# Optimization experiments

Measured on AMD Instinct MI355X. Metric: run time of the kernel, lower is better.

The kernel has to match this reference:

```python
import jax, jax.numpy as jnp
import numpy as np

MODEL_DIM = 2048
Q_HEADS = 32
KV_HEADS = 8
HEAD_DIM = MODEL_DIM // Q_HEADS  # 64
ROPE_BASE = 10000.0


def apply_rope(x, pos):
    # x: [B, S, H, D], interleaved-pair RoPE (torchtune-style)
    half = x.shape[-1] // 2
    inv_freq = 1.0 / (ROPE_BASE ** (jnp.arange(half, dtype=jnp.float32) * 2.0 / x.shape[-1]))
    ang = pos.astype(jnp.float32)[:, None] * inv_freq[None, :]        # [S, half]
    cos = jnp.cos(ang)[None, :, None, :]                              # [1,S,1,half]
    sin = jnp.sin(ang)[None, :, None, :]
    x1 = x[..., 0::2]
    x2 = x[..., 1::2]
    o1 = x1 * cos - x2 * sin
    o2 = x2 * cos + x1 * sin
    return jnp.stack([o1, o2], axis=-1).reshape(x.shape)


def setup_inputs() -> dict:
    key = jax.random.key(0)
    ks = jax.random.split(key, 5)
    B, S, D = 2, 2048, MODEL_DIM
    sd = 1.0 / np.sqrt(D)
    x = jax.random.normal(ks[0], (B, S, D), dtype=jnp.float32)
    wq = jax.random.normal(ks[1], (Q_HEADS * HEAD_DIM, D), dtype=jnp.float32) * sd
    wk = jax.random.normal(ks[2], (KV_HEADS * HEAD_DIM, D), dtype=jnp.float32) * sd
    wv = jax.random.normal(ks[3], (KV_HEADS * HEAD_DIM, D), dtype=jnp.float32) * sd
    wo = jax.random.normal(ks[4], (D, D), dtype=jnp.float32) * sd
    attention_mask = jnp.ones((B, S), dtype=bool)
    return {"x": x, "attention_mask": attention_mask, "wq": wq, "wk": wk, "wv": wv, "wo": wo}


def reference(x, attention_mask, wq, wk, wv, wo):
    B, S, D = x.shape
    rep = Q_HEADS // KV_HEADS
    q = (x @ wq.T).reshape(B, S, Q_HEADS, HEAD_DIM)
    k = (x @ wk.T).reshape(B, S, KV_HEADS, HEAD_DIM)
    v = (x @ wv.T).reshape(B, S, KV_HEADS, HEAD_DIM)
    # GQA repeat_interleave along head axis
    k = jnp.repeat(k, rep, axis=2)
    v = jnp.repeat(v, rep, axis=2)
    pos = jnp.arange(S)
    q = apply_rope(q, pos)
    k = apply_rope(k, pos)
    # scores [B, H, Sq, Sk]
    score = jnp.einsum('bqhd,bkhd->bhqk', q, k) / np.sqrt(HEAD_DIM)
    neg_inf = jnp.finfo(score.dtype).min
    causal = jnp.tril(jnp.ones((S, S), dtype=bool))
    score = jnp.where(causal[None, None, :, :], score, neg_inf)
    score = jnp.where(attention_mask[:, None, None, :], score, neg_inf)
    attn = jax.nn.softmax(score, axis=-1)
    out = jnp.einsum('bhqk,bkhd->bqhd', attn, v).reshape(B, S, D)
    return out @ wo.T
```

## Files before the change

### kernel.cpp

```cpp
#include <hip/hip_runtime.h>
#include <hip/hip_bf16.h>

#define S_LEN 2048
#define BATCH 2
#define DMODEL 2048
#define HQ 32
#define HKV 8
#define HD 64
#define NQ 2560
#define KDIM 2048

typedef __attribute__((ext_vector_type(8))) short bf16x8;
typedef __attribute__((ext_vector_type(4))) float f32x4;

#if __has_builtin(__builtin_amdgcn_exp2f)
#define EXP2(x) __builtin_amdgcn_exp2f(x)
#else
#define EXP2(x) exp2f(x)
#endif

template<int N> struct ic { static constexpr int value = N; };

static __device__ inline ushort f2bf(float f) {
    union { float f; unsigned u; } v; v.f = f;
    unsigned r = v.u + 0x7fff + ((v.u >> 16) & 1);
    return (ushort)(r >> 16);
}
static __device__ inline float bf2f(ushort h) {
    union { unsigned u; float f; } v; v.u = ((unsigned)h) << 16; return v.f;
}
static __device__ inline unsigned pack2(float lo, float hi) {
    return (unsigned)f2bf(lo) | ((unsigned)f2bf(hi) << 16);
}
static __device__ __forceinline__ unsigned pkbf(float lo, float hi) {
    union { float f; unsigned u; } a, b; a.f = lo; b.f = hi;
    return __builtin_amdgcn_perm(b.u + 0x8000u, a.u + 0x8000u, 0x07060302u);
}
static __device__ __forceinline__ unsigned cvtpk(float lo, float hi) {
    unsigned r;
    asm("v_cvt_pk_bf16_f32 %0, %1, %2" : "=v"(r) : "v"(lo), "v"(hi));
    return r;
}

static __device__ __forceinline__ void gload16(const ushort* g, ushort* l) {
    __builtin_amdgcn_global_load_lds(
        (const __attribute__((address_space(1))) unsigned int*)(g),
        (__attribute__((address_space(3))) unsigned int*)(l), 16, 0, 0);
}

#define BARRIER() asm volatile("s_barrier" ::: "memory")
#define WAITVM(N) asm volatile("s_waitcnt vmcnt(" #N ")" ::: "memory")

__global__ __launch_bounds__(256) void convert_kernel(const float* __restrict__ x,
                                                      const float* __restrict__ wq,
                                                      const float* __restrict__ wk,
                                                      const float* __restrict__ wv,
                                                      const float* __restrict__ wo,
                                                      ushort* __restrict__ xb,
                                                      ushort* __restrict__ wqkvb,
                                                      ushort* __restrict__ wob)
{
    size_t e = ((size_t)blockIdx.x * 256 + threadIdx.x) * 8;
    const float* src; ushort* dst;
    if (e < 8388608ul)       { src = x  + e;              dst = xb + e; }
    else if (e < 12582912ul) { src = wq + (e - 8388608);  dst = wqkvb + (e - 8388608); }
    else if (e < 13631488ul) { src = wk + (e - 12582912); dst = wqkvb + 4194304 + (e - 12582912); }
    else if (e < 14680064ul) { src = wv + (e - 13631488); dst = wqkvb + 5242880 + (e - 13631488); }
    else                     { src = wo + (e - 14680064); dst = wob + (e - 14680064); }
    float4 a = *(const float4*)src;
    float4 b = *(const float4*)(src + 4);
    uint4 p; p.x = pack2(a.x, a.y); p.y = pack2(a.z, a.w);
             p.z = pack2(b.x, b.y); p.w = pack2(b.z, b.w);
    *(uint4*)dst = p;
}

template<int BNF, int EPI>
__global__ __launch_bounds__(512, 2) void gemm256(const ushort* __restrict__ A,
                                                  const ushort* __restrict__ Bw,
                                                  ushort* __restrict__ qkv,
                                                  ushort* __restrict__ vT,
                                                  float* __restrict__ Cf)
{
    constexpr int BN = BNF * 64;
    constexpr int KT = KDIM / 64;
    __shared__ ushort As[2][256 * 64];
    __shared__ ushort Bs[2][BN * 64];
    const int t    = threadIdx.x;
    const int w    = t >> 6, lane = t & 63;
    const int quad = lane >> 4, l15 = lane & 15;
    const int l8   = lane >> 3;
    const int scw  = ((lane & 7) ^ (l8 & 7)) * 8;
    const int wm   = (w >> 2) * 128;
    const int wn   = (w & 3) * (BNF * 16);

    const int bid = blockIdx.x;
    const int sb  = (bid & 7) * 32 + (bid >> 3);
    const int mb  = (sb >> 4) * 256;
    const int nb  = (sb & 15) * BN;

    f32x4 acc[8][BNF] = {};
    bf16x8 a[4][2], b[BNF][2];

    auto SAH = [&](int buf, int half, int kb) {
        #pragma unroll
        for (int L = 0; L < 2; L++) {
            int r0 = half * 128 + (w * 2 + L) * 8;
            gload16(A + (size_t)(mb + r0 + l8) * KDIM + kb + scw, &As[buf][r0 * 64]);
        }
    };
    auto SB = [&](int buf, int kb) {
        #pragma unroll
        for (int L = 0; L < BNF; L++) {
            int r0 = (w * BNF + L) * 8;
            gload16(Bw + (size_t)(nb + r0 + l8) * KDIM + kb + scw, &Bs[buf][r0 * 64]);
        }
    };
    auto LA = [&](int buf, int hm) {
        #pragma unroll
        for (int i = 0; i < 4; i++) {
            int r = wm + hm * 64 + i * 16 + l15;
            int rs = r * 64, sw = r & 7;
            #pragma unroll
            for (int kc = 0; kc < 2; kc++)
                a[i][kc] = *(const bf16x8*)&As[buf][rs + (((kc << 2) | quad) ^ sw) * 8];
        }
    };
    auto LB = [&](int buf) {
        #pragma unroll
        for (int j = 0; j < BNF; j++) {
            int r = wn + j * 16 + l15;
            int rs = r * 64, sw = r & 7;
            #pragma unroll
            for (int kc = 0; kc < 2; kc++)
                b[j][kc] = *(const bf16x8*)&Bs[buf][rs + (((kc << 2) | quad) ^ sw) * 8];
        }
    };
    auto MM = [&](auto HM) {
        constexpr int hm = decltype(HM)::value;
        __builtin_amdgcn_s_setprio(1);
        #pragma unroll
        for (int i = 0; i < 4; i++)
            #pragma unroll
            for (int j = 0; j < BNF; j++) {
                f32x4 d = acc[hm * 4 + i][j];
                d = __builtin_amdgcn_mfma_f32_16x16x32_bf16(a[i][0], b[j][0], d, 0, 0, 0);
                d = __builtin_amdgcn_mfma_f32_16x16x32_bf16(a[i][1], b[j][1], d, 0, 0, 0);
                acc[hm * 4 + i][j] = d;
            }
        __builtin_amdgcn_s_setprio(0);
    };

    SAH(0, 0, 0); SAH(0, 1, 0); SB(0, 0);
    SAH(1, 0, 64); SB(1, 64);
    if constexpr (BNF == 3) WAITVM(5); else WAITVM(4);
    BARRIER();

    #pragma unroll 1
    for (int tt = 0; tt < KT - 2; tt++) {
        const int buf = tt & 1, o = buf ^ 1;
        LA(buf, 0); LB(buf);
        SAH(o, 1, (tt + 1) * 64);
        BARRIER();
        MM(ic<0>{});
        if constexpr (BNF == 3) WAITVM(7); else WAITVM(6);
        BARRIER();
        LA(buf, 1);
        SAH(buf, 0, (tt + 2) * 64); SB(buf, (tt + 2) * 64);
        BARRIER();
        MM(ic<1>{});
        if constexpr (BNF == 3) WAITVM(7); else WAITVM(6);
        BARRIER();
    }
    LA(0, 0); LB(0);
    SAH(1, 1, (KT - 1) * 64);
    BARRIER();
    MM(ic<0>{});
    if constexpr (BNF == 3) WAITVM(7); else WAITVM(6);
    BARRIER();
    LA(0, 1);
    BARRIER();
    MM(ic<1>{});
    WAITVM(2);
    BARRIER();
    LA(1, 0); LB(1);
    BARRIER();
    MM(ic<0>{});
    WAITVM(0);
    BARRIER();
    LA(1, 1);
    BARRIER();
    MM(ic<1>{});

    #pragma unroll
    for (int i = 0; i < 8; i++) {
        int m0 = mb + wm + (i >> 2) * 64 + (i & 3) * 16 + quad * 4;
        #pragma unroll
        for (int j = 0; j < BNF; j++) {
            int n0 = nb + wn + j * 16;
            if (EPI == 0) {
                if (n0 >= 2560) {
                    int m0p = (m0 & ~63) | (((m0 >> 5) & 1) << 5)
                            | (((m0 >> 2) & 3) << 3) | (((m0 >> 4) & 1) << 2);
                    ushort4 pk;
                    pk.x = f2bf(acc[i][j][0]); pk.y = f2bf(acc[i][j][1]);
                    pk.z = f2bf(acc[i][j][2]); pk.w = f2bf(acc[i][j][3]);
                    *(ushort4*)&vT[(size_t)(n0 + l15 - 2560) * 4096 + m0p] = pk;
                } else {
                    #pragma unroll
                    for (int r = 0; r < 4; r++)
                        qkv[(size_t)(m0 + r) * NQ + n0 + l15] = f2bf(acc[i][j][r]);
                }
            } else {
                #pragma unroll
                for (int r = 0; r < 4; r++)
                    Cf[(size_t)(m0 + r) * DMODEL + n0 + l15] = acc[i][j][r];
            }
        }
    }
}

__global__ __launch_bounds__(256) void rope_kernel(ushort* __restrict__ qkv)
{
    const int PAIRS = BATCH * S_LEN * (HQ + HKV) * (HD / 2);
    int tid = blockIdx.x * 256 + threadIdx.x;
    if (tid >= PAIRS) return;
    int token = tid / ((HQ + HKV) * 32);
    int r     = tid - token * ((HQ + HKV) * 32);
    int hh    = r >> 5;
    int i     = r & 31;
    int base  = (hh < HQ) ? hh * 64 : DMODEL + (hh - HQ) * 64;
    size_t addr = (size_t)token * NQ + base + 2 * i;
    int s = token & (S_LEN - 1);
    float freq = exp2f(-0.41524101186092f * (float)i);
    float ang  = (float)s * freq;
    float sn, cs;
    sincosf(ang, &sn, &cs);
    float x1 = bf2f(qkv[addr]);
    float x2 = bf2f(qkv[addr + 1]);
    qkv[addr]     = f2bf(x1 * cs - x2 * sn);
    qkv[addr + 1] = f2bf(x2 * cs + x1 * sn);
}

__global__ __launch_bounds__(256) void attn_kernel(const ushort* __restrict__ qkv,
                                                   const ushort* __restrict__ vT,
                                                   ushort* __restrict__ attnb)
{
    __shared__ ushort Ks[2][2 * 64 * 64];
    __shared__ ushort VT[2][2 * 64 * 64];
    const int t    = threadIdx.x;
    const int w    = t >> 6, lane = t & 63;
    const int quad = lane >> 4, l15 = lane & 15;
    const int bid  = blockIdx.x;
    const int qx   = 15 - (bid >> 6);
    const int h    = bid & 31;
    const int b    = (bid >> 5) & 1;
    const int qb   = qx * 128;
    const int kvh  = h >> 2;
    const ushort* base = qkv + (size_t)b * S_LEN * NQ;
    const ushort* vTb  = vT + (size_t)kvh * HD * 4096 + b * S_LEN;

    const float SC = 0.18033688011112042f;
    bf16x8 aq[2][2];
    #pragma unroll
    for (int h2 = 0; h2 < 2; h2++) {
        const ushort* qp = base + (size_t)(qb + w * 32 + h2 * 16 + l15) * NQ + h * HD + quad * 8;
        #pragma unroll
        for (int hf = 0; hf < 2; hf++) {
            bf16x8 v = *(const bf16x8*)(qp + hf * 32);
            #pragma unroll
            for (int j = 0; j < 8; j++) v[j] = (short)f2bf(bf2f((ushort)v[j]) * SC);
            aq[h2][hf] = v;
        }
    }

    f32x4 o[2][4] = {};
    float lsum[2] = {};
    const int qw    = qb + w * 32;
    const int strow = lane >> 3;
    const int stlc  = (lane & 7) ^ strow;
    const int niter = qx + 1;

    auto stage = [&](int i, int buf) {
        #pragma unroll
        for (int c = 0; c < 4; c++) {
            int key = w * 32 + c * 8 + strow;
            gload16(base + (size_t)(i * 128 + key) * NQ + DMODEL + kvh * HD + stlc * 8,
                    &Ks[buf][(w * 32 + c * 8) * 64]);
        }
        #pragma unroll
        for (int s = 0; s < 2; s++)
            #pragma unroll
            for (int c = 0; c < 2; c++) {
                int dr = w * 16 + c * 8 + strow;
                gload16(vTb + (size_t)dr * 4096 + i * 128 + s * 64 + stlc * 8,
                        &VT[buf][s * 4096 + (w * 16 + c * 8) * 64]);
            }
    };

    auto compute = [&](const ushort* ks, const ushort* vs, int kb) {
        const bool full = (kb + 63) <= qw;
        f32x4 s[2][4];
        __builtin_amdgcn_s_setprio(1);
        #pragma unroll
        for (int kt = 0; kt < 4; kt++) {
            int key = kt * 16 + l15;
            int sw  = l15 & 7;
            bf16x8 k0 = *(const bf16x8*)&ks[key * 64 + (quad ^ sw) * 8];
            bf16x8 k1 = *(const bf16x8*)&ks[key * 64 + (((quad + 4) & 7) ^ sw) * 8];
            #pragma unroll
            for (int h2 = 0; h2 < 2; h2++) {
                f32x4 z = {};
                z = __builtin_amdgcn_mfma_f32_16x16x32_bf16(k0, aq[h2][0], z, 0, 0, 0);
                z = __builtin_amdgcn_mfma_f32_16x16x32_bf16(k1, aq[h2][1], z, 0, 0, 0);
                s[h2][kt] = z;
            }
        }
        __builtin_amdgcn_s_setprio(0);
        bf16x8 pf[2][2];
        #pragma unroll
        for (int h2 = 0; h2 < 2; h2++) {
            union { unsigned u[8]; bf16x8 v[2]; } pw;
            #pragma unroll
            for (int kt = 0; kt < 4; kt++) {
                float p0 = EXP2(s[h2][kt][0]);
                float p1 = EXP2(s[h2][kt][1]);
                float p2 = EXP2(s[h2][kt][2]);
                float p3 = EXP2(s[h2][kt][3]);
                if (!full) {
                    int key0 = kb + kt * 16 + quad * 4;
                    int q    = qb + w * 32 + h2 * 16 + l15;
                    p0 = (key0 + 0 <= q) ? p0 : 0.f;
                    p1 = (key0 + 1 <= q) ? p1 : 0.f;
                    p2 = (key0 + 2 <= q) ? p2 : 0.f;
                    p3 = (key0 + 3 <= q) ? p3 : 0.f;
                }
                lsum[h2] += (p0 + p1) + (p2 + p3);
                pw.u[kt * 2 + 0] = cvtpk(p0, p1);
                pw.u[kt * 2 + 1] = cvtpk(p2, p3);
            }
            pf[h2][0] = pw.v[0];
            pf[h2][1] = pw.v[1];
        }
        __builtin_amdgcn_s_setprio(1);
        #pragma unroll
        for (int tt = 0; tt < 4; tt++) {
            int dr = tt * 16 + l15;
            int sw = l15 & 7;
            bf16x8 vf0 = *(const bf16x8*)&vs[dr * 64 + (quad ^ sw) * 8];
            bf16x8 vf1 = *(const bf16x8*)&vs[dr * 64 + (((quad + 4) & 7) ^ sw) * 8];
            #pragma unroll
            for (int h2 = 0; h2 < 2; h2++) {
                f32x4 oo = o[h2][tt];
                oo = __builtin_amdgcn_mfma_f32_16x16x32_bf16(vf0, pf[h2][0], oo, 0, 0, 0);
                oo = __builtin_amdgcn_mfma_f32_16x16x32_bf16(vf1, pf[h2][1], oo, 0, 0, 0);
                o[h2][tt] = oo;
            }
        }
        __builtin_amdgcn_s_setprio(0);
    };

    stage(0, 0);

    for (int i = 0; i < niter; i++) {
        const int cur = i & 1;
        WAITVM(0);
        BARRIER();
        if (i + 1 < niter) stage(i + 1, cur ^ 1);
        const int kb = i * 128;
        if (kb <= qw + 31)
            compute(&Ks[cur][0],    &VT[cur][0],    kb);
        if (kb + 64 <= qw + 31)
            compute(&Ks[cur][4096], &VT[cur][4096], kb + 64);
    }
    #pragma unroll
    for (int h2 = 0; h2 < 2; h2++) {
        float l = lsum[h2];
        l += __shfl_xor(l, 16, 64);
        l += __shfl_xor(l, 32, 64);
        float inv = 1.0f / l;
        ushort* ob = attnb + (size_t)(b * S_LEN + qb + w * 32 + h2 * 16 + l15) * DMODEL
                   + h * HD + quad * 4;
        #pragma unroll
        for (int tt = 0; tt < 4; tt++) {
            uint2 st;
            st.x = pkbf(o[h2][tt][0] * inv, o[h2][tt][1] * inv);
            st.y = pkbf(o[h2][tt][2] * inv, o[h2][tt][3] * inv);
            *(uint2*)&ob[tt * 16] = st;
        }
    }
}

extern "C" void kernel_launch(void* const* d_in, const int* in_sizes, int n_in,
                              void* d_out, int out_size, void* d_ws, size_t ws_size,
                              hipStream_t stream)
{
    const float* x  = (const float*)d_in[0];
    const float* wq = (const float*)d_in[2];
    const float* wk = (const float*)d_in[3];
    const float* wv = (const float*)d_in[4];
    const float* wo = (const float*)d_in[5];
    float* out = (float*)d_out;

    char* ws = (char*)d_ws;
    ushort* qkv    = (ushort*)(ws);
    ushort* vT     = (ushort*)(ws + 20971520);
    ushort* xb     = (ushort*)(ws + 25165824);
    ushort* attn_b = xb;
    ushort* wqkvb  = (ushort*)(ws + 41943040);
    ushort* wob    = (ushort*)(ws + 54525952);

    convert_kernel<<<9216, 256, 0, stream>>>(x, wq, wk, wv, wo, xb, wqkvb, wob);

    gemm256<3, 0><<<256, 512, 0, stream>>>(xb, wqkvb, qkv, vT, nullptr);

    int pairs = BATCH * S_LEN * (HQ + HKV) * (HD / 2);
    rope_kernel<<<(pairs + 255) / 256, 256, 0, stream>>>(qkv);

    attn_kernel<<<1024, 256, 0, stream>>>(qkv, vT, attn_b);

    gemm256<2, 1><<<256, 512, 0, stream>>>(attn_b, wob, nullptr, nullptr, out);
}
```

Before: 264.7 us.

## Fuse Q RoPE into attention loads and double query rows per block

The standalone RoPE pass now rotates only K. Q rotation moves into the attention kernel's Q load, where it is computed with sincos per element before scaling. Each attention block now covers 256 query rows (64 per wave) instead of 128, so every K/V tile staged in shared memory feeds twice as many MFMAs, and the grid is halved to 512 blocks. The score/softmax stage is restructured per key tile to limit live registers. The trade-off is higher register pressure, fewer blocks for load balancing under the causal mask, and more wasted masked work on diagonal tiles.

```diff
diff --git a/kernel.cpp b/kernel.cpp
--- a/kernel.cpp
+++ b/kernel.cpp
@@ -221,15 +221,14 @@
 
 __global__ __launch_bounds__(256) void rope_kernel(ushort* __restrict__ qkv)
 {
-    const int PAIRS = BATCH * S_LEN * (HQ + HKV) * (HD / 2);
+    const int PAIRS = BATCH * S_LEN * HKV * (HD / 2);
     int tid = blockIdx.x * 256 + threadIdx.x;
     if (tid >= PAIRS) return;
-    int token = tid / ((HQ + HKV) * 32);
-    int r     = tid - token * ((HQ + HKV) * 32);
+    int token = tid / (HKV * 32);
+    int r     = tid - token * (HKV * 32);
     int hh    = r >> 5;
     int i     = r & 31;
-    int base  = (hh < HQ) ? hh * 64 : DMODEL + (hh - HQ) * 64;
-    size_t addr = (size_t)token * NQ + base + 2 * i;
+    size_t addr = (size_t)token * NQ + DMODEL + hh * 64 + 2 * i;
     int s = token & (S_LEN - 1);
     float freq = exp2f(-0.41524101186092f * (float)i);
     float ang  = (float)s * freq;
@@ -251,34 +250,44 @@
     const int w    = t >> 6, lane = t & 63;
     const int quad = lane >> 4, l15 = lane & 15;
     const int bid  = blockIdx.x;
-    const int qx   = 15 - (bid >> 6);
+    const int qs   = 7 - (bid >> 6);
     const int h    = bid & 31;
     const int b    = (bid >> 5) & 1;
-    const int qb   = qx * 128;
+    const int qb   = qs * 256;
     const int kvh  = h >> 2;
     const ushort* base = qkv + (size_t)b * S_LEN * NQ;
     const ushort* vTb  = vT + (size_t)kvh * HD * 4096 + b * S_LEN;
 
     const float SC = 0.18033688011112042f;
-    bf16x8 aq[2][2];
+    bf16x8 aq[4][2];
     #pragma unroll
-    for (int h2 = 0; h2 < 2; h2++) {
-        const ushort* qp = base + (size_t)(qb + w * 32 + h2 * 16 + l15) * NQ + h * HD + quad * 8;
+    for (int h2 = 0; h2 < 4; h2++) {
+        const int row = qb + w * 64 + h2 * 16 + l15;
+        const ushort* qp = base + (size_t)row * NQ + h * HD + quad * 8;
         #pragma unroll
         for (int hf = 0; hf < 2; hf++) {
             bf16x8 v = *(const bf16x8*)(qp + hf * 32);
             #pragma unroll
-            for (int j = 0; j < 8; j++) v[j] = (short)f2bf(bf2f((ushort)v[j]) * SC);
+            for (int p = 0; p < 4; p++) {
+                int m = hf * 16 + quad * 4 + p;
+                float freq = exp2f(-0.41524101186092f * (float)m);
+                float sn, cs;
+                sincosf((float)row * freq, &sn, &cs);
+                float x1 = bf2f((ushort)v[2 * p]);
+                float x2 = bf2f((ushort)v[2 * p + 1]);
+                v[2 * p]     = (short)f2bf((x1 * cs - x2 * sn) * SC);
+                v[2 * p + 1] = (short)f2bf((x2 * cs + x1 * sn) * SC);
+            }
             aq[h2][hf] = v;
         }
     }
 
-    f32x4 o[2][4] = {};
-    float lsum[2] = {};
-    const int qw    = qb + w * 32;
+    f32x4 o[4][4] = {};
+    float lsum[4] = {};
+    const int qw    = qb + w * 64;
     const int strow = lane >> 3;
     const int stlc  = (lane & 7) ^ strow;
-    const int niter = qx + 1;
+    const int niter = (qb + 256) / 128;
 
     auto stage = [&](int i, int buf) {
         #pragma unroll
@@ -299,47 +308,41 @@
 
     auto compute = [&](const ushort* ks, const ushort* vs, int kb) {
         const bool full = (kb + 63) <= qw;
-        f32x4 s[2][4];
-        __builtin_amdgcn_s_setprio(1);
+        union { unsigned u[8]; bf16x8 v[2]; } pw[4];
         #pragma unroll
         for (int kt = 0; kt < 4; kt++) {
             int key = kt * 16 + l15;
             int sw  = l15 & 7;
             bf16x8 k0 = *(const bf16x8*)&ks[key * 64 + (quad ^ sw) * 8];
             bf16x8 k1 = *(const bf16x8*)&ks[key * 64 + (((quad + 4) & 7) ^ sw) * 8];
-            #pragma unroll
-            for (int h2 = 0; h2 < 2; h2++) {
+            f32x4 sx[4];
+            __builtin_amdgcn_s_setprio(1);
+            #pragma unroll
+            for (int h2 = 0; h2 < 4; h2++) {
                 f32x4 z = {};
                 z = __builtin_amdgcn_mfma_f32_16x16x32_bf16(k0, aq[h2][0], z, 0, 0, 0);
                 z = __builtin_amdgcn_mfma_f32_16x16x32_bf16(k1, aq[h2][1], z, 0, 0, 0);
-                s[h2][kt] = z;
-            }
-        }
-        __builtin_amdgcn_s_setprio(0);
-        bf16x8 pf[2][2];
-        #pragma unroll
-        for (int h2 = 0; h2 < 2; h2++) {
-            union { unsigned u[8]; bf16x8 v[2]; } pw;
-            #pragma unroll
-            for (int kt = 0; kt < 4; kt++) {
-                float p0 = EXP2(s[h2][kt][0]);
-                float p1 = EXP2(s[h2][kt][1]);
-                float p2 = EXP2(s[h2][kt][2]);
-                float p3 = EXP2(s[h2][kt][3]);
+                sx[h2] = z;
+            }
+            __builtin_amdgcn_s_setprio(0);
+            #pragma unroll
+            for (int h2 = 0; h2 < 4; h2++) {
+                float p0 = EXP2(sx[h2][0]);
+                float p1 = EXP2(sx[h2][1]);
+                float p2 = EXP2(sx[h2][2]);
+                float p3 = EXP2(sx[h2][3]);
                 if (!full) {
                     int key0 = kb + kt * 16 + quad * 4;
-                    int q    = qb + w * 32 + h2 * 16 + l15;
+                    int q    = qb + w * 64 + h2 * 16 + l15;
                     p0 = (key0 + 0 <= q) ? p0 : 0.f;
                     p1 = (key0 + 1 <= q) ? p1 : 0.f;
                     p2 = (key0 + 2 <= q) ? p2 : 0.f;
                     p3 = (key0 + 3 <= q) ? p3 : 0.f;
                 }
                 lsum[h2] += (p0 + p1) + (p2 + p3);
-                pw.u[kt * 2 + 0] = cvtpk(p0, p1);
-                pw.u[kt * 2 + 1] = cvtpk(p2, p3);
-            }
-            pf[h2][0] = pw.v[0];
-            pf[h2][1] = pw.v[1];
+                pw[h2].u[kt * 2 + 0] = cvtpk(p0, p1);
+                pw[h2].u[kt * 2 + 1] = cvtpk(p2, p3);
+            }
         }
         __builtin_amdgcn_s_setprio(1);
         #pragma unroll
@@ -349,10 +352,10 @@
             bf16x8 vf0 = *(const bf16x8*)&vs[dr * 64 + (quad ^ sw) * 8];
             bf16x8 vf1 = *(const bf16x8*)&vs[dr * 64 + (((quad + 4) & 7) ^ sw) * 8];
             #pragma unroll
-            for (int h2 = 0; h2 < 2; h2++) {
+            for (int h2 = 0; h2 < 4; h2++) {
                 f32x4 oo = o[h2][tt];
-                oo = __builtin_amdgcn_mfma_f32_16x16x32_bf16(vf0, pf[h2][0], oo, 0, 0, 0);
-                oo = __builtin_amdgcn_mfma_f32_16x16x32_bf16(vf1, pf[h2][1], oo, 0, 0, 0);
+                oo = __builtin_amdgcn_mfma_f32_16x16x32_bf16(vf0, pw[h2].v[0], oo, 0, 0, 0);
+                oo = __builtin_amdgcn_mfma_f32_16x16x32_bf16(vf1, pw[h2].v[1], oo, 0, 0, 0);
                 o[h2][tt] = oo;
             }
         }
@@ -367,18 +370,18 @@
         BARRIER();
         if (i + 1 < niter) stage(i + 1, cur ^ 1);
         const int kb = i * 128;
-        if (kb <= qw + 31)
+        if (kb <= qw + 63)
             compute(&Ks[cur][0],    &VT[cur][0],    kb);
-        if (kb + 64 <= qw + 31)
+        if (kb + 64 <= qw + 63)
             compute(&Ks[cur][4096], &VT[cur][4096], kb + 64);
     }
     #pragma unroll
-    for (int h2 = 0; h2 < 2; h2++) {
+    for (int h2 = 0; h2 < 4; h2++) {
         float l = lsum[h2];
         l += __shfl_xor(l, 16, 64);
         l += __shfl_xor(l, 32, 64);
         float inv = 1.0f / l;
-        ushort* ob = attnb + (size_t)(b * S_LEN + qb + w * 32 + h2 * 16 + l15) * DMODEL
+        ushort* ob = attnb + (size_t)(b * S_LEN + qb + w * 64 + h2 * 16 + l15) * DMODEL
                    + h * HD + quad * 4;
         #pragma unroll
         for (int tt = 0; tt < 4; tt++) {
@@ -413,10 +416,10 @@
 
     gemm256<3, 0><<<256, 512, 0, stream>>>(xb, wqkvb, qkv, vT, nullptr);
 
-    int pairs = BATCH * S_LEN * (HQ + HKV) * (HD / 2);
+    int pairs = BATCH * S_LEN * HKV * (HD / 2);
     rope_kernel<<<(pairs + 255) / 256, 256, 0, stream>>>(qkv);
 
-    attn_kernel<<<1024, 256, 0, stream>>>(qkv, vT, attn_b);
+    attn_kernel<<<512, 256, 0, stream>>>(qkv, vT, attn_b);
 
     gemm256<2, 1><<<256, 512, 0, stream>>>(attn_b, wob, nullptr, nullptr, out);
 }
```

Result: slower. 284.6 us (+7.5%).
